# Performance work log

Hardware: AMD Instinct MI355X
Metric: run time of the kernel (lower is better)

The kernel has to match this reference:

```python
import jax, jax.numpy as jnp
import numpy as np

BETA = 0.9
GAMMA = -0.1
EPSILON = 2.0
LAMBDA = 1e-4

B, COLS, FEAT, E = 16384, 32, 500000, 16
ACC = COLS * E          # 512
NE = 8                  # num_experts
SBH = 256               # SB_hidden
SBO = 128               # SB_output
TH = 16                 # towers_hidden
T = 2                   # num_tasks


def setup_inputs() -> dict:
    key = jax.random.key(0)
    ks = jax.random.split(key, 16)
    eps = 1e-4
    return {
        "x": jax.random.randint(ks[0], (B, COLS), 0, FEAT, dtype=jnp.int64 if jax.config.jax_enable_x64 else jnp.int32),
        "emb": jax.random.normal(ks[1], (FEAT, E), dtype=jnp.float32),
        "alpha1": jax.random.uniform(ks[2], (1,), minval=eps, maxval=1.0, dtype=jnp.float32),
        "u1": jax.random.uniform(ks[3], (ACC, NE, SBH), minval=eps, maxval=1.0 - eps, dtype=jnp.float32),
        "w1": jax.random.normal(ks[4], (ACC, NE, SBH), dtype=jnp.float32) * np.sqrt(2.0 / (ACC + SBH)),
        "alpha2": jax.random.uniform(ks[5], (1,), minval=eps, maxval=1.0, dtype=jnp.float32),
        "u2": jax.random.uniform(ks[6], (SBH, SBO), minval=eps, maxval=1.0 - eps, dtype=jnp.float32),
        "w2": jax.random.normal(ks[7], (SBH, SBO), dtype=jnp.float32) * np.sqrt(2.0 / (SBH + SBO)),
        "fce_w": jax.random.normal(ks[8], (1, NE), dtype=jnp.float32) * 0.1,
        "fce_b": jnp.zeros((1,), dtype=jnp.float32),
        "tw1": jax.random.normal(ks[9], (T, SBO, TH), dtype=jnp.float32) * np.sqrt(1.0 / SBO),
        "tb1": jnp.zeros((T, TH), dtype=jnp.float32),
        "tw2": jax.random.normal(ks[10], (T, TH, 1), dtype=jnp.float32) * np.sqrt(1.0 / TH),
        "tb2": jnp.zeros((T, 1), dtype=jnp.float32),
    }


def _hard_concrete(u, alpha):
    # s = sigmoid(log u - log(1-u) + log(alpha)/beta); s_ = s*(eps-gamma)+gamma
    s = jax.nn.sigmoid(jnp.log(u) - jnp.log(1.0 - u) + jnp.log(alpha) / BETA)
    s_ = s * (EPSILON - GAMMA) + GAMMA
    # z = (s_>0)*s_ then clamp above at 1  == clip(s_, 0, 1)
    z = jnp.clip(s_, 0.0, 1.0)
    return s_, z


def reference(x, emb, alpha1, u1, w1, alpha2, u2, w2, fce_w, fce_b, tw1, tb1, tw2, tb2):
    # embedding gather + field concat -> [B, COLS*E]
    xf = emb[x].reshape(x.shape[0], -1)
    s1_, z1 = _hard_concrete(u1, alpha1)
    o = jnp.einsum('ab,bnc->anc', xf, z1 * w1)          # [B, NE, SBH]
    s2_, z2 = _hard_concrete(u2, alpha2)
    o = jnp.einsum('anc,cd->and', o, z2 * w2)           # [B, NE, SBO]
    o = jnp.swapaxes(o, 1, 2)                           # [B, SBO, NE]
    o = o @ fce_w.T + fce_b                             # [B, SBO, 1]
    o = jax.nn.relu(jnp.squeeze(o, -1))                 # [B, SBO]
    # per-task towers (dropout is inference no-op)
    h = jax.nn.relu(jnp.einsum('bd,tdh->tbh', o, tw1) + tb1[:, None, :])
    outs = jax.nn.sigmoid(jnp.einsum('tbh,tho->tbo', h, tw2) + tb2[:, None, :])  # [T, B, 1]
    # L0-style regularizer (integer ops, zero gradient)
    s1_prob = 1 - (s1_ < 0).sum(axis=-1) // s1_.shape[1]
    s2_prob = 1 - (s2_ < 0).sum(axis=-1) // s2_.shape[1]
    regul = LAMBDA * (s1_prob.sum() + s2_prob.sum()).astype(jnp.float32)
    return outs, regul
```

## Files before the change

### kernel.cpp

```cpp
#include <hip/hip_runtime.h>
#include <hip/hip_bf16.h>
#include <math.h>

#define B_ROWS 16384
#define NCOLS 32
#define EDIM 16
#define ACCD 512
#define NE 8
#define SBH 256
#define SBO 128
#define THD 16
#define NT 2

#define ROWS 32
#define THR 512

typedef __attribute__((ext_vector_type(8))) short bf16x8;
typedef __attribute__((ext_vector_type(4))) float f32x4;
typedef __attribute__((ext_vector_type(16))) float f32x16;

__device__ __forceinline__ short f2bf(float f) {
    unsigned u = __float_as_uint(f);
    unsigned r = (u + 0x7FFFu + ((u >> 16) & 1u)) >> 16;
    return (short)r;
}

__device__ __forceinline__ bf16x8 pack8(float4 a, float4 b) {
    bf16x8 v;
    v[0] = f2bf(a.x); v[1] = f2bf(a.y); v[2] = f2bf(a.z); v[3] = f2bf(a.w);
    v[4] = f2bf(b.x); v[5] = f2bf(b.y); v[6] = f2bf(b.z); v[7] = f2bf(b.w);
    return v;
}


__global__ __launch_bounds__(256) void k_prep(const float* __restrict__ u1,
                                              const float* __restrict__ w1,
                                              const float* __restrict__ alpha1,
                                              const float* __restrict__ fce_w,
                                              const float* __restrict__ u2,
                                              const float* __restrict__ w2,
                                              const float* __restrict__ alpha2,
                                              const float* __restrict__ tw1,
                                              short* __restrict__ W1cT,
                                              short* __restrict__ W2T,
                                              short* __restrict__ tw1T,
                                              int* __restrict__ regparts) {
    const int bid = blockIdx.x;
    const int tid = threadIdx.x;
    if (bid < 512) {
        const int a = bid, c = tid;
        const float A = expf(-logf(alpha1[0]) * (1.0f / 0.9f));
        __shared__ int cnts[NE];
        if (c < NE) cnts[c] = 0;
        __syncthreads();
        float acc = 0.0f;
        #pragma unroll
        for (int n = 0; n < NE; ++n) {
            const int idx = (a * NE + n) * SBH + c;
            const float u = u1[idx];
            const float s = u / (u + (1.0f - u) * A);
            const float s_ = s * 2.1f - 0.1f;
            const float z = fminf(fmaxf(s_, 0.0f), 1.0f);
            acc += z * w1[idx] * fce_w[n];
            unsigned long long m = __ballot(s_ < 0.0f);
            if ((c & 63) == 0) atomicAdd(&cnts[n], __popcll(m));
        }
        __syncthreads();
        W1cT[c * ACCD + a] = f2bf(acc);
        if (c == 0) {
            int tot = 0;
            #pragma unroll
            for (int n = 0; n < NE; ++n) tot += 1 - cnts[n] / NE;
            regparts[a] = tot;
        }
    } else if (bid < 640) {
        const int c = (bid - 512) * 2 + (tid >> 7);
        const int d = tid & 127;
        const float A = expf(-logf(alpha2[0]) * (1.0f / 0.9f));
        const int idx = c * SBO + d;
        const float u = u2[idx];
        const float s = u / (u + (1.0f - u) * A);
        const float s_ = s * 2.1f - 0.1f;
        const float z = fminf(fmaxf(s_, 0.0f), 1.0f);
        W2T[d * SBH + c] = f2bf(z * w2[idx]);
        __shared__ int cnts2[2];
        if (tid < 2) cnts2[tid] = 0;
        __syncthreads();
        unsigned long long m = __ballot(s_ < 0.0f);
        if ((tid & 63) == 0) atomicAdd(&cnts2[tid >> 7], __popcll(m));
        __syncthreads();
        if ((tid & 127) == 0) regparts[ACCD + c] = 1 - cnts2[tid >> 7] / SBO;
    } else {
        #pragma unroll
        for (int i = 0; i < 16; ++i) {
            const int e = tid * 16 + i;
            const int jj = e >> 7;
            const int d = e & 127;
            tw1T[jj * SBO + d] = f2bf(tw1[((jj >> 4) * SBO + d) * THD + (jj & 15)]);
        }
    }
}

__global__ __launch_bounds__(THR, 4) void k_main(const int* __restrict__ x,
                                                 const float* __restrict__ emb,
                                                 const short* __restrict__ W1cT,
                                                 const short* __restrict__ W2T,
                                                 const short* __restrict__ tw1T,
                                                 const float* __restrict__ fce_b,
                                                 const float* __restrict__ tb1,
                                                 const float* __restrict__ tw2,
                                                 const float* __restrict__ tb2,
                                                 const int* __restrict__ regparts,
                                                 float* __restrict__ outp) {
    __shared__ __align__(16) char lds[32768];
    char* xfb = lds;
    char* tbuf = lds + 16384;
    char* ob = lds;

    const int tid = threadIdx.x;
    const int l = tid & 63;
    const int w = tid >> 6;
    const int rowbase = blockIdx.x * ROWS;
    const int lrow32 = l & 31;
    const int hg = l >> 5;
    const int lrow16 = l & 15;
    const int lg4 = (l >> 4) & 3;

    const int srow = tid >> 4;
    const int sseg = tid & 15;
    const int sswz = (srow & 15) << 4;
    char* sbase = xfb + (srow << 9);

    char* abase = xfb + (lrow32 << 9);
    const int aswz = (lrow32 & 15) << 4;

    f32x16 acc;
    #pragma unroll
    for (int i = 0; i < 16; ++i) acc[i] = 0.0f;

    for (int kb = 0; kb < 2; ++kb) {
        {
            const int xv = x[(rowbase + srow) * NCOLS + kb * 16 + sseg];
            const float4* ep = reinterpret_cast<const float4*>(emb + (size_t)xv * EDIM);
            const float4 e0 = ep[0], e1 = ep[1], e2 = ep[2], e3 = ep[3];
            *(bf16x8*)(sbase + ((sseg * 32 + 0) ^ sswz))  = pack8(e0, e1);
            *(bf16x8*)(sbase + ((sseg * 32 + 16) ^ sswz)) = pack8(e2, e3);
        }
        __syncthreads();
        const short* bptr = W1cT + (w * 32 + lrow32) * ACCD + kb * 256 + hg * 8;
        #pragma unroll
        for (int kc = 0; kc < 16; ++kc) {
            const bf16x8 av = *(const bf16x8*)(abase + ((kc * 32 + hg * 16) ^ aswz));
            const bf16x8 bv = *(const bf16x8*)(bptr + kc * 16);
            acc = __builtin_amdgcn_mfma_f32_32x32x16_bf16(av, bv, acc, 0, 0, 0);
        }
        __syncthreads();
    }

    {
        const int tcol2 = (w * 32 + lrow32) * 2;
        #pragma unroll
        for (int r = 0; r < 16; ++r) {
            const int trow = (r & 3) + 8 * (r >> 2) + 4 * hg;
            *(short*)(tbuf + (trow << 9) + (tcol2 ^ ((trow & 15) << 4))) = f2bf(acc[r]);
        }
    }
    __syncthreads();

    f32x4 acc2[2];
    acc2[0] = (f32x4){0.f, 0.f, 0.f, 0.f};
    acc2[1] = (f32x4){0.f, 0.f, 0.f, 0.f};
    {
        const int rA = (w >> 2) * 16 + lrow16;
        char* tAb = tbuf + (rA << 9);
        const int tswz = (rA & 15) << 4;
        const short* b2p = W2T + ((w & 3) * 32 + lrow16) * SBH + lg4 * 8;
        #pragma unroll
        for (int kc = 0; kc < 8; ++kc) {
            const bf16x8 av = *(const bf16x8*)(tAb + ((kc * 64 + lg4 * 16) ^ tswz));
            const bf16x8 b0 = *(const bf16x8*)(b2p + kc * 32);
            const bf16x8 b1 = *(const bf16x8*)(b2p + 16 * SBH + kc * 32);
            acc2[0] = __builtin_amdgcn_mfma_f32_16x16x32_bf16(av, b0, acc2[0], 0, 0, 0);
            acc2[1] = __builtin_amdgcn_mfma_f32_16x16x32_bf16(av, b1, acc2[1], 0, 0, 0);
        }
    }
    {
        const float fb = fce_b[0];
        const int rt2 = w >> 2, cg = w & 3;
        #pragma unroll
        for (int fd = 0; fd < 2; ++fd) {
            const int d2 = (cg * 32 + fd * 16 + lrow16) * 2;
            #pragma unroll
            for (int rr = 0; rr < 4; ++rr) {
                const int orow = rt2 * 16 + lg4 * 4 + rr;
                const float v = fmaxf(acc2[fd][rr] + fb, 0.0f);
                *(short*)(ob + (orow << 8) + (d2 ^ ((orow & 15) << 4))) = f2bf(v);
            }
        }
    }
    __syncthreads();

    if (w < 4) {
        const int rtt = w >> 1, ct = w & 1;
        f32x4 h = (f32x4){0.f, 0.f, 0.f, 0.f};
        char* oAb = ob + ((rtt * 16 + lrow16) << 8);
        const int oswz = ((rtt * 16 + lrow16) & 15) << 4;
        const short* bT = tw1T + (ct * 16 + lrow16) * SBO + lg4 * 8;
        #pragma unroll
        for (int kc = 0; kc < 4; ++kc) {
            const bf16x8 av = *(const bf16x8*)(oAb + ((kc * 64 + lg4 * 16) ^ oswz));
            const bf16x8 bv = *(const bf16x8*)(bT + kc * 32);
            h = __builtin_amdgcn_mfma_f32_16x16x32_bf16(av, bv, h, 0, 0, 0);
        }
        const float b1v = tb1[ct * THD + lrow16];
        const float w2v = tw2[ct * THD + lrow16];
        float p[4];
        #pragma unroll
        for (int rr = 0; rr < 4; ++rr) {
            p[rr] = fmaxf(h[rr] + b1v, 0.0f) * w2v;
            #pragma unroll
            for (int off = 8; off >= 1; off >>= 1)
                p[rr] += __shfl_xor(p[rr], off);
        }
        if (lrow16 == 0) {
            const float b2v = tb2[ct];
            #pragma unroll
            for (int rr = 0; rr < 4; ++rr) {
                const int rowo = rtt * 16 + lg4 * 4 + rr;
                outp[ct * B_ROWS + rowbase + rowo] = 1.0f / (1.0f + __expf(-(p[rr] + b2v)));
            }
        }
    }

    if (blockIdx.x == 0 && tid < 64) {
        int s = 0;
        for (int i = tid; i < ACCD + SBH; i += 64) s += regparts[i];
        #pragma unroll
        for (int off = 32; off > 0; off >>= 1) s += __shfl_down(s, off);
        if (tid == 0) outp[NT * B_ROWS] = 1e-4f * (float)s;
    }
}

extern "C" void kernel_launch(void* const* d_in, const int* in_sizes, int n_in,
                              void* d_out, int out_size, void* d_ws, size_t ws_size,
                              hipStream_t stream) {
    const int*   x      = (const int*)d_in[0];
    const float* emb    = (const float*)d_in[1];
    const float* alpha1 = (const float*)d_in[2];
    const float* u1     = (const float*)d_in[3];
    const float* w1     = (const float*)d_in[4];
    const float* alpha2 = (const float*)d_in[5];
    const float* u2     = (const float*)d_in[6];
    const float* w2     = (const float*)d_in[7];
    const float* fce_w  = (const float*)d_in[8];
    const float* fce_b  = (const float*)d_in[9];
    const float* tw1    = (const float*)d_in[10];
    const float* tb1    = (const float*)d_in[11];
    const float* tw2    = (const float*)d_in[12];
    const float* tb2    = (const float*)d_in[13];
    float* outp = (float*)d_out;

    short* W1cT = (short*)d_ws;
    short* W2T  = W1cT + SBH * ACCD;
    short* tw1T = W2T + SBO * SBH;
    int*   regparts = (int*)(tw1T + NT * THD * SBO);

    k_prep<<<641, 256, 0, stream>>>(u1, w1, alpha1, fce_w, u2, w2, alpha2, tw1,
                                    W1cT, W2T, tw1T, regparts);
    k_main<<<B_ROWS / ROWS, THR, 0, stream>>>(x, emb, W1cT, W2T, tw1T, fce_b,
                                              tb1, tw2, tb2, regparts, outp);
}
```

Before: 140.1 us.

## Process 64 rows per block with fragment-ordered weights and prefetched B operands

Doubles the rows handled per block from 32 to 64. The whole 32-column embedding gather is staged into LDS at once, and each wave computes two 32x32 MFMA tiles so every weight fragment is reused across more rows. The prep kernel now writes W1 and W2 in per-lane MFMA fragment order, so each lane loads contiguous 16-byte B operands, and those loads are software-prefetched four k-steps ahead. The second GEMM moves to 32x32 MFMA as well. In exchange the block uses 64KB of LDS and the launch bound drops to 2 blocks per CU, which lowers occupancy and latency hiding for the random embedding gathers.

```diff
diff --git a/kernel.cpp b/kernel.cpp
--- a/kernel.cpp
+++ b/kernel.cpp
@@ -12,7 +12,7 @@
 #define THD 16
 #define NT 2
 
-#define ROWS 32
+#define ROWS 64
 #define THR 512
 
 typedef __attribute__((ext_vector_type(8))) short bf16x8;
@@ -41,8 +41,8 @@
                                               const float* __restrict__ w2,
                                               const float* __restrict__ alpha2,
                                               const float* __restrict__ tw1,
-                                              short* __restrict__ W1cT,
-                                              short* __restrict__ W2T,
+                                              short* __restrict__ W1cF,
+                                              short* __restrict__ W2F,
                                               short* __restrict__ tw1T,
                                               int* __restrict__ regparts) {
     const int bid = blockIdx.x;
@@ -66,7 +66,12 @@
             if ((c & 63) == 0) atomicAdd(&cnts[n], __popcll(m));
         }
         __syncthreads();
-        W1cT[c * ACCD + a] = f2bf(acc);
+        {
+            const int ks = a >> 4, kr = a & 15;
+            const int sub = kr >> 3, j = kr & 7;
+            const int cg = c >> 5, lane = (sub << 5) | (c & 31);
+            W1cF[(((ks * 8 + cg) * 64) + lane) * 8 + j] = f2bf(acc);
+        }
         if (c == 0) {
             int tot = 0;
             #pragma unroll
@@ -82,7 +87,12 @@
         const float s = u / (u + (1.0f - u) * A);
         const float s_ = s * 2.1f - 0.1f;
         const float z = fminf(fmaxf(s_, 0.0f), 1.0f);
-        W2T[d * SBH + c] = f2bf(z * w2[idx]);
+        {
+            const int ks = c >> 4, kr = c & 15;
+            const int sub = kr >> 3, j = kr & 7;
+            const int cg = d >> 5, lane = (sub << 5) | (d & 31);
+            W2F[(((ks * 4 + cg) * 64) + lane) * 8 + j] = f2bf(z * w2[idx]);
+        }
         __shared__ int cnts2[2];
         if (tid < 2) cnts2[tid] = 0;
         __syncthreads();
@@ -101,10 +111,12 @@
     }
 }
 
-__global__ __launch_bounds__(THR, 4) void k_main(const int* __restrict__ x,
+#define MFMA32(a, b, c) __builtin_amdgcn_mfma_f32_32x32x16_bf16((a), (b), (c), 0, 0, 0)
+
+__global__ __launch_bounds__(THR, 2) void k_main(const int* __restrict__ x,
                                                  const float* __restrict__ emb,
-                                                 const short* __restrict__ W1cT,
-                                                 const short* __restrict__ W2T,
+                                                 const short* __restrict__ W1cF,
+                                                 const short* __restrict__ W2F,
                                                  const short* __restrict__ tw1T,
                                                  const float* __restrict__ fce_b,
                                                  const float* __restrict__ tb1,
@@ -112,99 +124,144 @@
                                                  const float* __restrict__ tb2,
                                                  const int* __restrict__ regparts,
                                                  float* __restrict__ outp) {
-    __shared__ __align__(16) char lds[32768];
-    char* xfb = lds;
-    char* tbuf = lds + 16384;
-    char* ob = lds;
+    __shared__ __align__(16) char lds[65536];
 
     const int tid = threadIdx.x;
     const int l = tid & 63;
     const int w = tid >> 6;
-    const int rowbase = blockIdx.x * ROWS;
     const int lrow32 = l & 31;
     const int hg = l >> 5;
     const int lrow16 = l & 15;
     const int lg4 = (l >> 4) & 3;
-
-    const int srow = tid >> 4;
-    const int sseg = tid & 15;
-    const int sswz = (srow & 15) << 4;
-    char* sbase = xfb + (srow << 9);
-
-    char* abase = xfb + (lrow32 << 9);
-    const int aswz = (lrow32 & 15) << 4;
-
-    f32x16 acc;
+    const int rowbase = blockIdx.x * ROWS;
+
+    {
+        const int r0 = tid >> 3;
+        const int cb = (tid & 7) * 4;
+        const int4 xv4 = *reinterpret_cast<const int4*>(x + (rowbase + r0) * NCOLS + cb);
+        char* rbase = lds + (r0 << 10);
+        const int swz = (r0 & 15) << 4;
+        int xs[4] = {xv4.x, xv4.y, xv4.z, xv4.w};
+        #pragma unroll
+        for (int i = 0; i < 4; ++i) {
+            const float4* ep = reinterpret_cast<const float4*>(emb + (size_t)xs[i] * EDIM);
+            const float4 e0 = ep[0], e1 = ep[1], e2 = ep[2], e3 = ep[3];
+            *(bf16x8*)(rbase + ((((cb + i) * 32) + 0) ^ swz))  = pack8(e0, e1);
+            *(bf16x8*)(rbase + ((((cb + i) * 32) + 16) ^ swz)) = pack8(e2, e3);
+        }
+    }
+    __syncthreads();
+
+    const int rg = w >> 2;
+    const int cgp = (w & 3) * 2;
+    f32x16 acc0, acc1;
     #pragma unroll
-    for (int i = 0; i < 16; ++i) acc[i] = 0.0f;
-
-    for (int kb = 0; kb < 2; ++kb) {
-        {
-            const int xv = x[(rowbase + srow) * NCOLS + kb * 16 + sseg];
-            const float4* ep = reinterpret_cast<const float4*>(emb + (size_t)xv * EDIM);
-            const float4 e0 = ep[0], e1 = ep[1], e2 = ep[2], e3 = ep[3];
-            *(bf16x8*)(sbase + ((sseg * 32 + 0) ^ sswz))  = pack8(e0, e1);
-            *(bf16x8*)(sbase + ((sseg * 32 + 16) ^ sswz)) = pack8(e2, e3);
-        }
-        __syncthreads();
-        const short* bptr = W1cT + (w * 32 + lrow32) * ACCD + kb * 256 + hg * 8;
-        #pragma unroll
-        for (int kc = 0; kc < 16; ++kc) {
-            const bf16x8 av = *(const bf16x8*)(abase + ((kc * 32 + hg * 16) ^ aswz));
-            const bf16x8 bv = *(const bf16x8*)(bptr + kc * 16);
-            acc = __builtin_amdgcn_mfma_f32_32x32x16_bf16(av, bv, acc, 0, 0, 0);
-        }
-        __syncthreads();
-    }
-
-    {
-        const int tcol2 = (w * 32 + lrow32) * 2;
+    for (int i = 0; i < 16; ++i) { acc0[i] = 0.0f; acc1[i] = 0.0f; }
+    {
+        char* aAb = lds + ((rg * 32 + lrow32) << 10);
+        const int aswz = (lrow32 & 15) << 4;
+        const bf16x8* Bp = ((const bf16x8*)W1cF) + l;
+
+        bf16x8 p0a = Bp[(0 * 8 + cgp) * 64], p0b = Bp[(0 * 8 + cgp + 1) * 64];
+        bf16x8 p1a = Bp[(1 * 8 + cgp) * 64], p1b = Bp[(1 * 8 + cgp + 1) * 64];
+        bf16x8 p2a = Bp[(2 * 8 + cgp) * 64], p2b = Bp[(2 * 8 + cgp + 1) * 64];
+        bf16x8 p3a = Bp[(3 * 8 + cgp) * 64], p3b = Bp[(3 * 8 + cgp + 1) * 64];
+
+        #pragma unroll
+        for (int ks = 0; ks < 32; ks += 4) {
+            {
+                const bf16x8 a = *(const bf16x8*)(aAb + ((((ks + 0) * 32) + hg * 16) ^ aswz));
+                acc0 = MFMA32(a, p0a, acc0);
+                acc1 = MFMA32(a, p0b, acc1);
+                if (ks + 4 < 32) { p0a = Bp[((ks + 4) * 8 + cgp) * 64]; p0b = Bp[((ks + 4) * 8 + cgp + 1) * 64]; }
+            }
+            {
+                const bf16x8 a = *(const bf16x8*)(aAb + ((((ks + 1) * 32) + hg * 16) ^ aswz));
+                acc0 = MFMA32(a, p1a, acc0);
+                acc1 = MFMA32(a, p1b, acc1);
+                if (ks + 5 < 32) { p1a = Bp[((ks + 5) * 8 + cgp) * 64]; p1b = Bp[((ks + 5) * 8 + cgp + 1) * 64]; }
+            }
+            {
+                const bf16x8 a = *(const bf16x8*)(aAb + ((((ks + 2) * 32) + hg * 16) ^ aswz));
+                acc0 = MFMA32(a, p2a, acc0);
+                acc1 = MFMA32(a, p2b, acc1);
+                if (ks + 6 < 32) { p2a = Bp[((ks + 6) * 8 + cgp) * 64]; p2b = Bp[((ks + 6) * 8 + cgp + 1) * 64]; }
+            }
+            {
+                const bf16x8 a = *(const bf16x8*)(aAb + ((((ks + 3) * 32) + hg * 16) ^ aswz));
+                acc0 = MFMA32(a, p3a, acc0);
+                acc1 = MFMA32(a, p3b, acc1);
+                if (ks + 7 < 32) { p3a = Bp[((ks + 7) * 8 + cgp) * 64]; p3b = Bp[((ks + 7) * 8 + cgp + 1) * 64]; }
+            }
+        }
+    }
+    __syncthreads();
+
+    {
         #pragma unroll
         for (int r = 0; r < 16; ++r) {
-            const int trow = (r & 3) + 8 * (r >> 2) + 4 * hg;
-            *(short*)(tbuf + (trow << 9) + (tcol2 ^ ((trow & 15) << 4))) = f2bf(acc[r]);
+            const int trow = rg * 32 + (r & 3) + 8 * (r >> 2) + 4 * hg;
+            const int sw = (trow & 15) << 4;
+            *(short*)(lds + (trow << 9) + ((((cgp * 32 + lrow32) * 2)) ^ sw)) = f2bf(acc0[r]);
+            *(short*)(lds + (trow << 9) + (((((cgp + 1) * 32 + lrow32) * 2)) ^ sw)) = f2bf(acc1[r]);
+        }
+    }
+
+    const int cg2 = w & 3;
+    f32x16 acc2;
+    #pragma unroll
+    for (int i = 0; i < 16; ++i) acc2[i] = 0.0f;
+    {
+        const bf16x8* Bp2 = ((const bf16x8*)W2F) + l;
+        bf16x8 q0 = Bp2[(0 * 4 + cg2) * 64];
+        bf16x8 q1 = Bp2[(1 * 4 + cg2) * 64];
+        bf16x8 q2 = Bp2[(2 * 4 + cg2) * 64];
+        bf16x8 q3 = Bp2[(3 * 4 + cg2) * 64];
+        __syncthreads();
+        char* tAb = lds + ((rg * 32 + lrow32) << 9);
+        const int tswz = (lrow32 & 15) << 4;
+        #pragma unroll
+        for (int ks = 0; ks < 16; ks += 4) {
+            {
+                const bf16x8 a = *(const bf16x8*)(tAb + ((((ks + 0) * 32) + hg * 16) ^ tswz));
+                acc2 = MFMA32(a, q0, acc2);
+                if (ks + 4 < 16) q0 = Bp2[((ks + 4) * 4 + cg2) * 64];
+            }
+            {
+                const bf16x8 a = *(const bf16x8*)(tAb + ((((ks + 1) * 32) + hg * 16) ^ tswz));
+                acc2 = MFMA32(a, q1, acc2);
+                if (ks + 5 < 16) q1 = Bp2[((ks + 5) * 4 + cg2) * 64];
+            }
+            {
+                const bf16x8 a = *(const bf16x8*)(tAb + ((((ks + 2) * 32) + hg * 16) ^ tswz));
+                acc2 = MFMA32(a, q2, acc2);
+                if (ks + 6 < 16) q2 = Bp2[((ks + 6) * 4 + cg2) * 64];
+            }
+            {
+                const bf16x8 a = *(const bf16x8*)(tAb + ((((ks + 3) * 32) + hg * 16) ^ tswz));
+                acc2 = MFMA32(a, q3, acc2);
+                if (ks + 7 < 16) q3 = Bp2[((ks + 7) * 4 + cg2) * 64];
+            }
+        }
+    }
+
+    {
+        const float fb = fce_b[0];
+        #pragma unroll
+        for (int r = 0; r < 16; ++r) {
+            const int orow = rg * 32 + (r & 3) + 8 * (r >> 2) + 4 * hg;
+            const int oc2 = (cg2 * 32 + lrow32) * 2;
+            *(short*)(lds + 32768 + (orow << 8) + (oc2 ^ ((orow & 15) << 4))) =
+                f2bf(fmaxf(acc2[r] + fb, 0.0f));
         }
     }
     __syncthreads();
 
-    f32x4 acc2[2];
-    acc2[0] = (f32x4){0.f, 0.f, 0.f, 0.f};
-    acc2[1] = (f32x4){0.f, 0.f, 0.f, 0.f};
-    {
-        const int rA = (w >> 2) * 16 + lrow16;
-        char* tAb = tbuf + (rA << 9);
-        const int tswz = (rA & 15) << 4;
-        const short* b2p = W2T + ((w & 3) * 32 + lrow16) * SBH + lg4 * 8;
-        #pragma unroll
-        for (int kc = 0; kc < 8; ++kc) {
-            const bf16x8 av = *(const bf16x8*)(tAb + ((kc * 64 + lg4 * 16) ^ tswz));
-            const bf16x8 b0 = *(const bf16x8*)(b2p + kc * 32);
-            const bf16x8 b1 = *(const bf16x8*)(b2p + 16 * SBH + kc * 32);
-            acc2[0] = __builtin_amdgcn_mfma_f32_16x16x32_bf16(av, b0, acc2[0], 0, 0, 0);
-            acc2[1] = __builtin_amdgcn_mfma_f32_16x16x32_bf16(av, b1, acc2[1], 0, 0, 0);
-        }
-    }
-    {
-        const float fb = fce_b[0];
-        const int rt2 = w >> 2, cg = w & 3;
-        #pragma unroll
-        for (int fd = 0; fd < 2; ++fd) {
-            const int d2 = (cg * 32 + fd * 16 + lrow16) * 2;
-            #pragma unroll
-            for (int rr = 0; rr < 4; ++rr) {
-                const int orow = rt2 * 16 + lg4 * 4 + rr;
-                const float v = fmaxf(acc2[fd][rr] + fb, 0.0f);
-                *(short*)(ob + (orow << 8) + (d2 ^ ((orow & 15) << 4))) = f2bf(v);
-            }
-        }
-    }
-    __syncthreads();
-
-    if (w < 4) {
+    {
         const int rtt = w >> 1, ct = w & 1;
         f32x4 h = (f32x4){0.f, 0.f, 0.f, 0.f};
-        char* oAb = ob + ((rtt * 16 + lrow16) << 8);
-        const int oswz = ((rtt * 16 + lrow16) & 15) << 4;
+        char* oAb = lds + 32768 + ((rtt * 16 + lrow16) << 8);
+        const int oswz = (lrow16 & 15) << 4;
         const short* bT = tw1T + (ct * 16 + lrow16) * SBO + lg4 * 8;
         #pragma unroll
         for (int kc = 0; kc < 4; ++kc) {
@@ -260,13 +317,13 @@
     const float* tb2    = (const float*)d_in[13];
     float* outp = (float*)d_out;
 
-    short* W1cT = (short*)d_ws;
-    short* W2T  = W1cT + SBH * ACCD;
-    short* tw1T = W2T + SBO * SBH;
+    short* W1cF = (short*)d_ws;
+    short* W2F  = W1cF + 32 * 8 * 64 * 8;
+    short* tw1T = W2F + 16 * 4 * 64 * 8;
     int*   regparts = (int*)(tw1T + NT * THD * SBO);
 
     k_prep<<<641, 256, 0, stream>>>(u1, w1, alpha1, fce_w, u2, w2, alpha2, tw1,
-                                    W1cT, W2T, tw1T, regparts);
-    k_main<<<B_ROWS / ROWS, THR, 0, stream>>>(x, emb, W1cT, W2T, tw1T, fce_b,
+                                    W1cF, W2F, tw1T, regparts);
+    k_main<<<B_ROWS / ROWS, THR, 0, stream>>>(x, emb, W1cF, W2F, tw1T, fce_b,
                                               tb1, tw2, tb2, regparts, outp);
 }
```

After: 126.4 us. -9.8%, faster.

## Pre-swizzle weights into MFMA fragment layout and overlap embedding gather with MMA

Applied to the files above, without the earlier changes.

The prep kernel now writes W1 and W2 in a fragment-major layout, so each lane reads its bf16x8 B operand with one fully coalesced 16-byte load. The main kernel issues both halves of the embedding gather up front and holds the second half in registers while the first-half MFMAs run. It also software-pipelines the B-operand loads four steps ahead and uses separate LDS regions so one barrier is dropped. The cost is LDS growing from 32 KB to 56 KB per block plus extra registers, which can lower occupancy below the launch-bounds target.

```diff
diff --git a/kernel.cpp b/kernel.cpp
--- a/kernel.cpp
+++ b/kernel.cpp
@@ -41,8 +41,8 @@
                                               const float* __restrict__ w2,
                                               const float* __restrict__ alpha2,
                                               const float* __restrict__ tw1,
-                                              short* __restrict__ W1cT,
-                                              short* __restrict__ W2T,
+                                              short* __restrict__ W1cF,
+                                              short* __restrict__ W2F,
                                               short* __restrict__ tw1T,
                                               int* __restrict__ regparts) {
     const int bid = blockIdx.x;
@@ -66,7 +66,12 @@
             if ((c & 63) == 0) atomicAdd(&cnts[n], __popcll(m));
         }
         __syncthreads();
-        W1cT[c * ACCD + a] = f2bf(acc);
+        {
+            const int ks = a >> 4, kr = a & 15;
+            const int sub = kr >> 3, j = kr & 7;
+            const int cg = c >> 5, lane = (sub << 5) | (c & 31);
+            W1cF[(((ks * 8 + cg) * 64) + lane) * 8 + j] = f2bf(acc);
+        }
         if (c == 0) {
             int tot = 0;
             #pragma unroll
@@ -82,7 +87,12 @@
         const float s = u / (u + (1.0f - u) * A);
         const float s_ = s * 2.1f - 0.1f;
         const float z = fminf(fmaxf(s_, 0.0f), 1.0f);
-        W2T[d * SBH + c] = f2bf(z * w2[idx]);
+        {
+            const int ks = c >> 5, krem = c & 31;
+            const int sub = krem >> 3, j = krem & 7;
+            const int cg = d >> 4, lane = (sub << 4) | (d & 15);
+            W2F[(((ks * 8 + cg) * 64) + lane) * 8 + j] = f2bf(z * w2[idx]);
+        }
         __shared__ int cnts2[2];
         if (tid < 2) cnts2[tid] = 0;
         __syncthreads();
@@ -101,10 +111,16 @@
     }
 }
 
+#define MFMA32(a, b, c) __builtin_amdgcn_mfma_f32_32x32x16_bf16((a), (b), (c), 0, 0, 0)
+#define MFMA16(a, b, c) __builtin_amdgcn_mfma_f32_16x16x32_bf16((a), (b), (c), 0, 0, 0)
+
+#define LDS_T 32768
+#define LDS_O 49152
+
 __global__ __launch_bounds__(THR, 4) void k_main(const int* __restrict__ x,
                                                  const float* __restrict__ emb,
-                                                 const short* __restrict__ W1cT,
-                                                 const short* __restrict__ W2T,
+                                                 const short* __restrict__ W1cF,
+                                                 const short* __restrict__ W2F,
                                                  const short* __restrict__ tw1T,
                                                  const float* __restrict__ fce_b,
                                                  const float* __restrict__ tb1,
@@ -112,57 +128,87 @@
                                                  const float* __restrict__ tb2,
                                                  const int* __restrict__ regparts,
                                                  float* __restrict__ outp) {
-    __shared__ __align__(16) char lds[32768];
-    char* xfb = lds;
-    char* tbuf = lds + 16384;
-    char* ob = lds;
+    __shared__ __align__(16) char lds[57344];
 
     const int tid = threadIdx.x;
     const int l = tid & 63;
     const int w = tid >> 6;
-    const int rowbase = blockIdx.x * ROWS;
     const int lrow32 = l & 31;
     const int hg = l >> 5;
     const int lrow16 = l & 15;
     const int lg4 = (l >> 4) & 3;
+    const int rowbase = blockIdx.x * ROWS;
 
     const int srow = tid >> 4;
-    const int sseg = tid & 15;
+    const int scol = tid & 15;
+    char* sbase = lds + (srow << 10);
     const int sswz = (srow & 15) << 4;
-    char* sbase = xfb + (srow << 9);
-
-    char* abase = xfb + (lrow32 << 9);
+
+    const int xv0 = x[(rowbase + srow) * NCOLS + scol];
+    const int xv1 = x[(rowbase + srow) * NCOLS + 16 + scol];
+
+    {
+        const float4* ep = reinterpret_cast<const float4*>(emb + (size_t)xv0 * EDIM);
+        const float4 e0 = ep[0], e1 = ep[1], e2 = ep[2], e3 = ep[3];
+        *(bf16x8*)(sbase + ((scol * 32 + 0) ^ sswz))  = pack8(e0, e1);
+        *(bf16x8*)(sbase + ((scol * 32 + 16) ^ sswz)) = pack8(e2, e3);
+    }
+    const float4* ep1 = reinterpret_cast<const float4*>(emb + (size_t)xv1 * EDIM);
+    const float4 g0 = ep1[0], g1 = ep1[1], g2 = ep1[2], g3 = ep1[3];
+    __syncthreads();
+
+    char* aAb = lds + (lrow32 << 10);
     const int aswz = (lrow32 & 15) << 4;
+    const bf16x8* Bp = ((const bf16x8*)W1cF) + l;
 
     f32x16 acc;
     #pragma unroll
     for (int i = 0; i < 16; ++i) acc[i] = 0.0f;
 
-    for (int kb = 0; kb < 2; ++kb) {
-        {
-            const int xv = x[(rowbase + srow) * NCOLS + kb * 16 + sseg];
-            const float4* ep = reinterpret_cast<const float4*>(emb + (size_t)xv * EDIM);
-            const float4 e0 = ep[0], e1 = ep[1], e2 = ep[2], e3 = ep[3];
-            *(bf16x8*)(sbase + ((sseg * 32 + 0) ^ sswz))  = pack8(e0, e1);
-            *(bf16x8*)(sbase + ((sseg * 32 + 16) ^ sswz)) = pack8(e2, e3);
-        }
-        __syncthreads();
-        const short* bptr = W1cT + (w * 32 + lrow32) * ACCD + kb * 256 + hg * 8;
-        #pragma unroll
-        for (int kc = 0; kc < 16; ++kc) {
-            const bf16x8 av = *(const bf16x8*)(abase + ((kc * 32 + hg * 16) ^ aswz));
-            const bf16x8 bv = *(const bf16x8*)(bptr + kc * 16);
-            acc = __builtin_amdgcn_mfma_f32_32x32x16_bf16(av, bv, acc, 0, 0, 0);
-        }
-        __syncthreads();
-    }
+    bf16x8 b0 = Bp[(0 * 8 + w) * 64];
+    bf16x8 b1 = Bp[(1 * 8 + w) * 64];
+    bf16x8 b2 = Bp[(2 * 8 + w) * 64];
+    bf16x8 b3 = Bp[(3 * 8 + w) * 64];
+
+    #pragma unroll
+    for (int ks = 0; ks < 16; ks += 4) {
+        { const bf16x8 a = *(const bf16x8*)(aAb + ((((ks + 0) * 32) + hg * 16) ^ aswz));
+          acc = MFMA32(a, b0, acc); b0 = Bp[((ks + 4) * 8 + w) * 64]; }
+        { const bf16x8 a = *(const bf16x8*)(aAb + ((((ks + 1) * 32) + hg * 16) ^ aswz));
+          acc = MFMA32(a, b1, acc); b1 = Bp[((ks + 5) * 8 + w) * 64]; }
+        { const bf16x8 a = *(const bf16x8*)(aAb + ((((ks + 2) * 32) + hg * 16) ^ aswz));
+          acc = MFMA32(a, b2, acc); b2 = Bp[((ks + 6) * 8 + w) * 64]; }
+        { const bf16x8 a = *(const bf16x8*)(aAb + ((((ks + 3) * 32) + hg * 16) ^ aswz));
+          acc = MFMA32(a, b3, acc); b3 = Bp[((ks + 7) * 8 + w) * 64]; }
+    }
+    *(bf16x8*)(sbase + (((16 + scol) * 32 + 0) ^ sswz))  = pack8(g0, g1);
+    *(bf16x8*)(sbase + (((16 + scol) * 32 + 16) ^ sswz)) = pack8(g2, g3);
+    __syncthreads();
+
+    #pragma unroll
+    for (int ks = 16; ks < 32; ks += 4) {
+        { const bf16x8 a = *(const bf16x8*)(aAb + ((((ks + 0) * 32) + hg * 16) ^ aswz));
+          acc = MFMA32(a, b0, acc); if (ks + 4 < 32) b0 = Bp[((ks + 4) * 8 + w) * 64]; }
+        { const bf16x8 a = *(const bf16x8*)(aAb + ((((ks + 1) * 32) + hg * 16) ^ aswz));
+          acc = MFMA32(a, b1, acc); if (ks + 5 < 32) b1 = Bp[((ks + 5) * 8 + w) * 64]; }
+        { const bf16x8 a = *(const bf16x8*)(aAb + ((((ks + 2) * 32) + hg * 16) ^ aswz));
+          acc = MFMA32(a, b2, acc); if (ks + 6 < 32) b2 = Bp[((ks + 6) * 8 + w) * 64]; }
+        { const bf16x8 a = *(const bf16x8*)(aAb + ((((ks + 3) * 32) + hg * 16) ^ aswz));
+          acc = MFMA32(a, b3, acc); if (ks + 7 < 32) b3 = Bp[((ks + 7) * 8 + w) * 64]; }
+    }
+
+    const int cgA = (w & 3) * 2;
+    const int rg2 = w >> 2;
+    const bf16x8* Bp2 = ((const bf16x8*)W2F) + l;
+    bf16x8 q0a = Bp2[(0 * 8 + cgA) * 64], q0b = Bp2[(0 * 8 + cgA + 1) * 64];
+    bf16x8 q1a = Bp2[(1 * 8 + cgA) * 64], q1b = Bp2[(1 * 8 + cgA + 1) * 64];
 
     {
         const int tcol2 = (w * 32 + lrow32) * 2;
         #pragma unroll
         for (int r = 0; r < 16; ++r) {
             const int trow = (r & 3) + 8 * (r >> 2) + 4 * hg;
-            *(short*)(tbuf + (trow << 9) + (tcol2 ^ ((trow & 15) << 4))) = f2bf(acc[r]);
+            *(short*)(lds + LDS_T + (trow << 9) + (tcol2 ^ ((trow & 15) << 4))) = f2bf(acc[r]);
         }
     }
     __syncthreads();
@@ -171,30 +217,31 @@
     acc2[0] = (f32x4){0.f, 0.f, 0.f, 0.f};
     acc2[1] = (f32x4){0.f, 0.f, 0.f, 0.f};
     {
-        const int rA = (w >> 2) * 16 + lrow16;
-        char* tAb = tbuf + (rA << 9);
-        const int tswz = (rA & 15) << 4;
-        const short* b2p = W2T + ((w & 3) * 32 + lrow16) * SBH + lg4 * 8;
-        #pragma unroll
-        for (int kc = 0; kc < 8; ++kc) {
-            const bf16x8 av = *(const bf16x8*)(tAb + ((kc * 64 + lg4 * 16) ^ tswz));
-            const bf16x8 b0 = *(const bf16x8*)(b2p + kc * 32);
-            const bf16x8 b1 = *(const bf16x8*)(b2p + 16 * SBH + kc * 32);
-            acc2[0] = __builtin_amdgcn_mfma_f32_16x16x32_bf16(av, b0, acc2[0], 0, 0, 0);
-            acc2[1] = __builtin_amdgcn_mfma_f32_16x16x32_bf16(av, b1, acc2[1], 0, 0, 0);
-        }
-    }
+        char* tAb = lds + LDS_T + ((rg2 * 16 + lrow16) << 9);
+        const int tswz = (lrow16 & 15) << 4;
+        #pragma unroll
+        for (int kc = 0; kc < 8; kc += 2) {
+            { const bf16x8 a = *(const bf16x8*)(tAb + ((((kc + 0) * 64) + lg4 * 16) ^ tswz));
+              acc2[0] = MFMA16(a, q0a, acc2[0]);
+              acc2[1] = MFMA16(a, q0b, acc2[1]);
+              if (kc + 2 < 8) { q0a = Bp2[((kc + 2) * 8 + cgA) * 64]; q0b = Bp2[((kc + 2) * 8 + cgA + 1) * 64]; } }
+            { const bf16x8 a = *(const bf16x8*)(tAb + ((((kc + 1) * 64) + lg4 * 16) ^ tswz));
+              acc2[0] = MFMA16(a, q1a, acc2[0]);
+              acc2[1] = MFMA16(a, q1b, acc2[1]);
+              if (kc + 3 < 8) { q1a = Bp2[((kc + 3) * 8 + cgA) * 64]; q1b = Bp2[((kc + 3) * 8 + cgA + 1) * 64]; } }
+        }
+    }
+
     {
         const float fb = fce_b[0];
-        const int rt2 = w >> 2, cg = w & 3;
         #pragma unroll
         for (int fd = 0; fd < 2; ++fd) {
-            const int d2 = (cg * 32 + fd * 16 + lrow16) * 2;
+            const int d2 = ((cgA + fd) * 16 + lrow16) * 2;
             #pragma unroll
             for (int rr = 0; rr < 4; ++rr) {
-                const int orow = rt2 * 16 + lg4 * 4 + rr;
-                const float v = fmaxf(acc2[fd][rr] + fb, 0.0f);
-                *(short*)(ob + (orow << 8) + (d2 ^ ((orow & 15) << 4))) = f2bf(v);
+                const int orow = rg2 * 16 + lg4 * 4 + rr;
+                *(short*)(lds + LDS_O + (orow << 8) + (d2 ^ ((orow & 15) << 4))) =
+                    f2bf(fmaxf(acc2[fd][rr] + fb, 0.0f));
             }
         }
     }
@@ -203,14 +250,14 @@
     if (w < 4) {
         const int rtt = w >> 1, ct = w & 1;
         f32x4 h = (f32x4){0.f, 0.f, 0.f, 0.f};
-        char* oAb = ob + ((rtt * 16 + lrow16) << 8);
-        const int oswz = ((rtt * 16 + lrow16) & 15) << 4;
+        char* oAb = lds + LDS_O + ((rtt * 16 + lrow16) << 8);
+        const int oswz = (lrow16 & 15) << 4;
         const short* bT = tw1T + (ct * 16 + lrow16) * SBO + lg4 * 8;
         #pragma unroll
         for (int kc = 0; kc < 4; ++kc) {
             const bf16x8 av = *(const bf16x8*)(oAb + ((kc * 64 + lg4 * 16) ^ oswz));
             const bf16x8 bv = *(const bf16x8*)(bT + kc * 32);
-            h = __builtin_amdgcn_mfma_f32_16x16x32_bf16(av, bv, h, 0, 0, 0);
+            h = MFMA16(av, bv, h);
         }
         const float b1v = tb1[ct * THD + lrow16];
         const float w2v = tw2[ct * THD + lrow16];
@@ -260,13 +307,13 @@
     const float* tb2    = (const float*)d_in[13];
     float* outp = (float*)d_out;
 
-    short* W1cT = (short*)d_ws;
-    short* W2T  = W1cT + SBH * ACCD;
-    short* tw1T = W2T + SBO * SBH;
+    short* W1cF = (short*)d_ws;
+    short* W2F  = W1cF + 32 * 8 * 64 * 8;
+    short* tw1T = W2F + 8 * 8 * 64 * 8;
     int*   regparts = (int*)(tw1T + NT * THD * SBO);
 
     k_prep<<<641, 256, 0, stream>>>(u1, w1, alpha1, fce_w, u2, w2, alpha2, tw1,
-                                    W1cT, W2T, tw1T, regparts);
-    k_main<<<B_ROWS / ROWS, THR, 0, stream>>>(x, emb, W1cT, W2T, tw1T, fce_b,
+                                    W1cF, W2F, tw1T, regparts);
+    k_main<<<B_ROWS / ROWS, THR, 0, stream>>>(x, emb, W1cF, W2F, tw1T, fce_b,
                                               tb1, tw2, tb2, regparts, outp);
 }
```

Result: faster. 123.0 us (-12.2%).
